# Optimization experiments

Measured on AMD Instinct MI355X. Metric: run time of the kernel, lower is better.

Reference implementation:

```python
import jax, jax.numpy as jnp
import numpy as np

N = 100000          # nodes
E = 1600000         # edges (before self-loops)
F_IN = 128          # dataset.num_node_features
HID = 32            # hidden_channels
HEADS = 4
NUM_CLASSES = 40
NEG_SLOPE = 0.2     # PyG GATConv default


def setup_inputs() -> dict:
    key = jax.random.key(0)
    ks = jax.random.split(key, 16)
    x = jax.random.normal(ks[0], (N, F_IN), dtype=jnp.float32)
    edge_index = jax.random.randint(ks[1], (2, E), 0, N, dtype=jnp.int64)

    def glorot(k, shape):
        lim = float(np.sqrt(6.0 / (shape[0] + shape[-1])))
        return jax.random.uniform(k, shape, jnp.float32, -lim, lim)

    # layer 0: F_IN -> HID, heads=HEADS, concat
    W0 = glorot(ks[2], (F_IN, HEADS * HID))
    as0 = glorot(ks[3], (HEADS, HID))
    ad0 = glorot(ks[4], (HEADS, HID))
    b0 = jnp.zeros((HEADS * HID,), jnp.float32)
    # layer 1: HEADS*HID -> HID, heads=HEADS, concat
    W1 = glorot(ks[5], (HEADS * HID, HEADS * HID))
    as1 = glorot(ks[6], (HEADS, HID))
    ad1 = glorot(ks[7], (HEADS, HID))
    b1 = jnp.zeros((HEADS * HID,), jnp.float32)
    # layer 2: HEADS*HID -> HID, heads=1, no concat
    W2 = glorot(ks[8], (HEADS * HID, HID))
    as2 = glorot(ks[9], (1, HID))
    ad2 = glorot(ks[10], (1, HID))
    b2 = jnp.zeros((HID,), jnp.float32)
    # final linear HID -> NUM_CLASSES
    lin_w = glorot(ks[11], (HID, NUM_CLASSES))
    lin_b = jnp.zeros((NUM_CLASSES,), jnp.float32)
    return dict(x=x, edge_index=edge_index, W0=W0, as0=as0, ad0=ad0, b0=b0,
                W1=W1, as1=as1, ad1=ad1, b1=b1,
                W2=W2, as2=as2, ad2=ad2, b2=b2, lin_w=lin_w, lin_b=lin_b)


def gat_conv(x, src, dst, W, a_src, a_dst, b, heads, out_ch, concat):
    n = x.shape[0]
    h = (x @ W).reshape(n, heads, out_ch)               # [N,H,C]
    alpha_s = (h * a_src).sum(-1)                        # [N,H]
    alpha_d = (h * a_dst).sum(-1)                        # [N,H]
    e = jax.nn.leaky_relu(alpha_s[src] + alpha_d[dst], NEG_SLOPE)  # [E,H]
    m = jax.ops.segment_max(e, dst, num_segments=n)      # segment softmax over in-edges
    e = jnp.exp(e - m[dst])
    denom = jax.ops.segment_sum(e, dst, num_segments=n)
    alpha = e / (denom[dst] + 1e-16)                     # [E,H]
    out = jax.ops.segment_sum(h[src] * alpha[:, :, None], dst, num_segments=n)  # [N,H,C]
    out = out.reshape(n, heads * out_ch) if concat else out.mean(axis=1)
    return out + b


def reference(x, edge_index, W0, as0, ad0, b0, W1, as1, ad1, b1,
              W2, as2, ad2, b2, lin_w, lin_b):
    n = x.shape[0]
    loop = jnp.arange(n, dtype=edge_index.dtype)
    src = jnp.concatenate([edge_index[0], loop])   # PyG GATConv adds self-loops
    dst = jnp.concatenate([edge_index[1], loop])
    x = jax.nn.relu(gat_conv(x, src, dst, W0, as0, ad0, b0, HEADS, HID, True))
    x = jax.nn.relu(gat_conv(x, src, dst, W1, as1, ad1, b1, HEADS, HID, True))
    x = jax.nn.relu(gat_conv(x, src, dst, W2, as2, ad2, b2, 1, HID, False))
    return x @ lin_w + lin_b
```

## Files before the change

kernel.cpp:

```cpp
#include <hip/hip_runtime.h>
#include <hip/hip_bf16.h>
#include <hip/hip_fp16.h>
#include <math.h>


#define NEG_SLOPE 0.2f

typedef __attribute__((ext_vector_type(8))) _Float16 f16x8;
typedef __attribute__((ext_vector_type(4))) float    f32x4;

struct h4pack { __half2 a, b; };


__global__ void zero1_kernel(int* __restrict__ a, int n) {
    int i = blockIdx.x * blockDim.x + threadIdx.x;
    if (i < n) a[i] = 0;
}

__global__ void count_rank_kernel(const int* __restrict__ ei, int eraw, int n,
                                  int* __restrict__ deg, int* __restrict__ rank) {
    int i = blockIdx.x * blockDim.x + threadIdx.x;
    int etot = eraw + n;
    if (i >= etot) return;
    int dst = (i < eraw) ? ei[eraw + i] : (i - eraw);
    rank[i] = atomicAdd(&deg[dst], 1);
}

__global__ __launch_bounds__(1024)
void scan_local_kernel(const int* __restrict__ deg, int* __restrict__ rowptr,
                       int* __restrict__ bsum, int n) {
    __shared__ int buf[1024];
    int tid = threadIdx.x;
    int i = blockIdx.x * 1024 + tid;
    int v = (i < n) ? deg[i] : 0;
    buf[tid] = v;
    __syncthreads();
    for (int off = 1; off < 1024; off <<= 1) {
        int t = (tid >= off) ? buf[tid - off] : 0;
        __syncthreads();
        buf[tid] += t;
        __syncthreads();
    }
    if (i < n) rowptr[i] = buf[tid] - v;
    if (tid == 1023) bsum[blockIdx.x] = buf[1023];
}

__global__ __launch_bounds__(128)
void scan_sums_kernel(const int* __restrict__ bsum, int* __restrict__ boffs, int nb) {
    __shared__ int buf[128];
    int tid = threadIdx.x;
    int v = (tid < nb) ? bsum[tid] : 0;
    buf[tid] = v;
    __syncthreads();
    for (int off = 1; off < 128; off <<= 1) {
        int t = (tid >= off) ? buf[tid - off] : 0;
        __syncthreads();
        buf[tid] += t;
        __syncthreads();
    }
    if (tid < nb) boffs[tid] = buf[tid] - v;
}

__global__ void scan_add_kernel(int* __restrict__ rowptr, const int* __restrict__ boffs,
                                int n, int etot) {
    int i = blockIdx.x * blockDim.x + threadIdx.x;
    if (i < n) rowptr[i] += boffs[i >> 10];
    if (i == 0) rowptr[n] = etot;
}

__global__ void scatter2_kernel(const int* __restrict__ ei, const int* __restrict__ rank,
                                int eraw, int n, const int* __restrict__ rowptr,
                                int* __restrict__ csr_src) {
    int i = blockIdx.x * blockDim.x + threadIdx.x;
    int etot = eraw + n;
    if (i >= etot) return;
    int src, dst;
    if (i < eraw) { src = ei[i]; dst = ei[eraw + i]; }
    else          { src = i - eraw; dst = src; }
    csr_src[rowptr[dst] + rank[i]] = src;
}


template <int OUTC>
__global__ void wpack_f16_kernel(const float* __restrict__ W, __half* __restrict__ Wp) {
    int i = blockIdx.x * blockDim.x + threadIdx.x;
    int j    = i & 7;
    int lane = (i >> 3) & 63;
    int ks   = (i >> 9) & 3;
    int ct   = i >> 11;
    int k = ks * 32 + (lane >> 4) * 8 + j;
    int c = ct * 16 + (lane & 15);
    Wp[i] = __float2half(W[k * OUTC + c]);
}


template <bool F32IN>
__global__ __launch_bounds__(256)
void gemm_mfma_coef_kernel(const void* __restrict__ Xv, const __half* __restrict__ Wp,
                           const float* __restrict__ a_s, const float* __restrict__ a_d,
                           __half* __restrict__ H, float* __restrict__ as_out,
                           float* __restrict__ ad_out, int n) {
    int t = threadIdx.x;
    int lane = t & 63;
    int wave = t >> 6;
    int l15 = lane & 15;
    int kg  = lane >> 4;
    int wbase = blockIdx.x * 128 + wave * 32;

    int node0 = wbase + l15;
    int node1 = wbase + 16 + l15;
    int n0c = (node0 < n) ? node0 : 0;
    int n1c = (node1 < n) ? node1 : 0;

    f32x4 acc[2][8];
#pragma unroll
    for (int tt = 0; tt < 2; tt++)
#pragma unroll
        for (int i = 0; i < 8; i++) acc[tt][i] = (f32x4){0.f, 0.f, 0.f, 0.f};

#pragma unroll
    for (int ks = 0; ks < 4; ks++) {
        f16x8 b0, b1;
        if constexpr (F32IN) {
            const float* X = (const float*)Xv;
            const float* p0 = X + (size_t)n0c * 128 + kg * 8 + ks * 32;
            const float* p1 = X + (size_t)n1c * 128 + kg * 8 + ks * 32;
            float4 x0 = *(const float4*)(p0), x1 = *(const float4*)(p0 + 4);
            b0[0] = (_Float16)x0.x; b0[1] = (_Float16)x0.y; b0[2] = (_Float16)x0.z; b0[3] = (_Float16)x0.w;
            b0[4] = (_Float16)x1.x; b0[5] = (_Float16)x1.y; b0[6] = (_Float16)x1.z; b0[7] = (_Float16)x1.w;
            float4 y0 = *(const float4*)(p1), y1 = *(const float4*)(p1 + 4);
            b1[0] = (_Float16)y0.x; b1[1] = (_Float16)y0.y; b1[2] = (_Float16)y0.z; b1[3] = (_Float16)y0.w;
            b1[4] = (_Float16)y1.x; b1[5] = (_Float16)y1.y; b1[6] = (_Float16)y1.z; b1[7] = (_Float16)y1.w;
        } else {
            const __half* X = (const __half*)Xv;
            b0 = *(const f16x8*)(X + (size_t)n0c * 128 + kg * 8 + ks * 32);
            b1 = *(const f16x8*)(X + (size_t)n1c * 128 + kg * 8 + ks * 32);
        }
#pragma unroll
        for (int ct = 0; ct < 8; ct++) {
            f16x8 a = *(const f16x8*)(Wp + (size_t)((ct * 4 + ks) * 64 + lane) * 8);
            acc[0][ct] = __builtin_amdgcn_mfma_f32_16x16x32_f16(a, b0, acc[0][ct], 0, 0, 0);
            acc[1][ct] = __builtin_amdgcn_mfma_f32_16x16x32_f16(a, b1, acc[1][ct], 0, 0, 0);
        }
    }

#pragma unroll
    for (int tt = 0; tt < 2; tt++) {
        int node = wbase + tt * 16 + l15;
        if (node < n) {
#pragma unroll
            for (int ct = 0; ct < 8; ct++) {
                h4pack p;
                p.a = __floats2half2_rn(acc[tt][ct][0], acc[tt][ct][1]);
                p.b = __floats2half2_rn(acc[tt][ct][2], acc[tt][ct][3]);
                *(h4pack*)(H + (size_t)node * 128 + ct * 16 + kg * 4) = p;
            }
        }
    }

#pragma unroll
    for (int tt = 0; tt < 2; tt++) {
        int node = wbase + tt * 16 + l15;
#pragma unroll
        for (int h = 0; h < 4; h++) {
            float s = 0.f, d = 0.f;
#pragma unroll
            for (int q = 0; q < 2; q++) {
                int ct = 2 * h + q;
#pragma unroll
                for (int r = 0; r < 4; r++) {
                    int c = q * 16 + kg * 4 + r;
                    float v = acc[tt][ct][r];
                    s += v * a_s[h * 32 + c];
                    d += v * a_d[h * 32 + c];
                }
            }
            s += __shfl_xor(s, 16); s += __shfl_xor(s, 32);
            d += __shfl_xor(d, 16); d += __shfl_xor(d, 32);
            if (kg == 0 && node < n) {
                as_out[(size_t)node * 4 + h] = s;
                ad_out[(size_t)node * 4 + h] = d;
            }
        }
    }
}


__global__ __launch_bounds__(256)
void gemm_mfma_l2_kernel(const __half* __restrict__ X, const __half* __restrict__ Wp,
                         const float* __restrict__ a_s, const float* __restrict__ a_d,
                         __half* __restrict__ H, float* __restrict__ as_out,
                         float* __restrict__ ad_out, int n) {
    __shared__ __half hs[4][32][40];
    int t = threadIdx.x;
    int wave = t >> 6, lane = t & 63;
    int l15 = lane & 15;
    int kg  = lane >> 4;
    int wbase = blockIdx.x * 128 + wave * 32;

    int row0 = wbase + l15;
    int row1 = wbase + 16 + l15;
    int r0c = (row0 < n) ? row0 : 0;
    int r1c = (row1 < n) ? row1 : 0;

    f32x4 acc[2][2];
#pragma unroll
    for (int tt = 0; tt < 2; tt++)
#pragma unroll
        for (int i = 0; i < 2; i++) acc[tt][i] = (f32x4){0.f, 0.f, 0.f, 0.f};

#pragma unroll
    for (int ks = 0; ks < 4; ks++) {
        f16x8 a0 = *(const f16x8*)(X + (size_t)r0c * 128 + kg * 8 + ks * 32);
        f16x8 a1 = *(const f16x8*)(X + (size_t)r1c * 128 + kg * 8 + ks * 32);
#pragma unroll
        for (int ct = 0; ct < 2; ct++) {
            f16x8 b = *(const f16x8*)(Wp + (size_t)((ct * 4 + ks) * 64 + lane) * 8);
            acc[0][ct] = __builtin_amdgcn_mfma_f32_16x16x32_f16(a0, b, acc[0][ct], 0, 0, 0);
            acc[1][ct] = __builtin_amdgcn_mfma_f32_16x16x32_f16(a1, b, acc[1][ct], 0, 0, 0);
        }
    }

#pragma unroll
    for (int tt = 0; tt < 2; tt++)
#pragma unroll
        for (int ct = 0; ct < 2; ct++)
#pragma unroll
            for (int r = 0; r < 4; r++)
                hs[wave][tt * 16 + kg * 4 + r][ct * 16 + l15] = __float2half(acc[tt][ct][r]);
    __syncthreads();

#pragma unroll
    for (int it = 0; it < 2; it++) {
        int lr    = it * 16 + (lane >> 2);
        int chunk = lane & 3;
        int orow  = wbase + lr;
        if (orow < n) {
            uint4 v = *(const uint4*)&hs[wave][lr][chunk * 8];
            *(uint4*)(H + (size_t)orow * 32 + chunk * 8) = v;
        }
    }

    if (lane < 32) {
        int orow = wbase + lane;
        if (orow < n) {
            const __half2* hp = (const __half2*)&hs[wave][lane][0];
            float s = 0.f, d = 0.f;
#pragma unroll
            for (int c2 = 0; c2 < 16; c2++) {
                float2 v = __half22float2(hp[c2]);
                s += v.x * a_s[2 * c2] + v.y * a_s[2 * c2 + 1];
                d += v.x * a_d[2 * c2] + v.y * a_d[2 * c2 + 1];
            }
            as_out[orow] = s;
            ad_out[orow] = d;
        }
    }
}


__global__ __launch_bounds__(256)
void gat_fused_f16_kernel(const __half* __restrict__ Hm,
                          const float* __restrict__ as_,
                          const float* __restrict__ ad_,
                          const int* __restrict__ rowptr,
                          const int* __restrict__ csr,
                          const float* __restrict__ bias,
                          __half* __restrict__ out, int n) {
    constexpr int GS = 32;
    int t = threadIdx.x;
    int node = blockIdx.x * 8 + (t >> 5);
    if (node >= n) return;
    int tl = t & 31;
    int h  = tl >> 3;
    int k8 = tl & 7;
    const uint2* H8 = (const uint2*)Hm;
    int e0 = rowptr[node], e1 = rowptr[node + 1];
    float ad_d = ad_[(size_t)node * 4 + h];

    int  ce  = e0 + k8;
    bool vA  = ce < e1;
    int  idxA = vA ? csr[ce] : 0;
    float asA = vA ? as_[(size_t)idxA * 4 + h] : 0.f;

    float m = -INFINITY, l = 0.f;
    float4 acc = make_float4(0.f, 0.f, 0.f, 0.f);

    for (int eb = e0; eb < e1; eb += 8) {
        uint2 u[8];
#pragma unroll
        for (int j = 0; j < 8; j++) {
            int src = __shfl(idxA, j, 8);
            u[j] = H8[(size_t)src * GS + tl];
        }

        int  ne  = eb + 8 + k8;
        bool vB  = ne < e1;
        int  idxB = vB ? csr[ne] : 0;
        float asB = vB ? as_[(size_t)idxB * 4 + h] : 0.f;

        float el = asA + ad_d;
        el = (el > 0.f) ? el : NEG_SLOPE * el;
        el = vA ? el : -INFINITY;

        float cm = el;
        cm = fmaxf(cm, __shfl_xor(cm, 1, 8));
        cm = fmaxf(cm, __shfl_xor(cm, 2, 8));
        cm = fmaxf(cm, __shfl_xor(cm, 4, 8));
        float m_new = fmaxf(m, cm);
        float scale = __expf(m - m_new);
        float p = vA ? __expf(el - m_new) : 0.f;

        float ps = p;
        ps += __shfl_xor(ps, 1, 8);
        ps += __shfl_xor(ps, 2, 8);
        ps += __shfl_xor(ps, 4, 8);
        l = l * scale + ps;
        acc.x *= scale; acc.y *= scale; acc.z *= scale; acc.w *= scale;
        m = m_new;

#pragma unroll
        for (int j = 0; j < 8; j++) {
            float pj  = __shfl(p, j, 8);
            float2 f01 = __half22float2(*(const __half2*)&u[j].x);
            float2 f23 = __half22float2(*(const __half2*)&u[j].y);
            acc.x += pj * f01.x; acc.y += pj * f01.y;
            acc.z += pj * f23.x; acc.w += pj * f23.y;
        }
        idxA = idxB; asA = asB; vA = vB;
    }

    float li = 1.f / (l + 1e-16f);
    float4 b4 = ((const float4*)bias)[tl];
    float4 o;
    o.x = fmaxf(acc.x * li + b4.x, 0.f);
    o.y = fmaxf(acc.y * li + b4.y, 0.f);
    o.z = fmaxf(acc.z * li + b4.z, 0.f);
    o.w = fmaxf(acc.w * li + b4.w, 0.f);
    h4pack po;
    po.a = __floats2half2_rn(o.x, o.y);
    po.b = __floats2half2_rn(o.z, o.w);
    ((h4pack*)out)[(size_t)node * 32 + tl] = po;
}


__global__ __launch_bounds__(256)
void gat_fused_l2_kernel(const __half* __restrict__ Hm,
                         const float* __restrict__ as_,
                         const float* __restrict__ ad_,
                         const int* __restrict__ rowptr,
                         const int* __restrict__ csr,
                         const float* __restrict__ bias,
                         const float* __restrict__ lw,
                         const float* __restrict__ lb,
                         float* __restrict__ out, int n) {
    int t = threadIdx.x;
    int node = blockIdx.x * 32 + (t >> 3);
    if (node >= n) return;
    int tl = t & 7;
    const uint2* H8 = (const uint2*)Hm;
    int e0 = rowptr[node], e1 = rowptr[node + 1];
    float ad_d = ad_[node];

    int  ce  = e0 + tl;
    bool vA  = ce < e1;
    int  idxA = vA ? csr[ce] : 0;
    float asA = vA ? as_[idxA] : 0.f;

    float m = -INFINITY, l = 0.f;
    float4 acc = make_float4(0.f, 0.f, 0.f, 0.f);

    for (int eb = e0; eb < e1; eb += 8) {
        uint2 u[8];
#pragma unroll
        for (int j = 0; j < 8; j++) {
            int src = __shfl(idxA, j, 8);
            u[j] = H8[(size_t)src * 8 + tl];
        }

        int  ne  = eb + 8 + tl;
        bool vB  = ne < e1;
        int  idxB = vB ? csr[ne] : 0;
        float asB = vB ? as_[idxB] : 0.f;

        float el = asA + ad_d;
        el = (el > 0.f) ? el : NEG_SLOPE * el;
        el = vA ? el : -INFINITY;

        float cm = el;
        cm = fmaxf(cm, __shfl_xor(cm, 1, 8));
        cm = fmaxf(cm, __shfl_xor(cm, 2, 8));
        cm = fmaxf(cm, __shfl_xor(cm, 4, 8));
        float m_new = fmaxf(m, cm);
        float scale = __expf(m - m_new);
        float p = vA ? __expf(el - m_new) : 0.f;

        float ps = p;
        ps += __shfl_xor(ps, 1, 8);
        ps += __shfl_xor(ps, 2, 8);
        ps += __shfl_xor(ps, 4, 8);
        l = l * scale + ps;
        acc.x *= scale; acc.y *= scale; acc.z *= scale; acc.w *= scale;
        m = m_new;

#pragma unroll
        for (int j = 0; j < 8; j++) {
            float pj  = __shfl(p, j, 8);
            float2 f01 = __half22float2(*(const __half2*)&u[j].x);
            float2 f23 = __half22float2(*(const __half2*)&u[j].y);
            acc.x += pj * f01.x; acc.y += pj * f01.y;
            acc.z += pj * f23.x; acc.w += pj * f23.y;
        }
        idxA = idxB; asA = asB; vA = vB;
    }

    float li = 1.f / (l + 1e-16f);
    float4 b4 = ((const float4*)bias)[tl];
    float4 o;
    o.x = fmaxf(acc.x * li + b4.x, 0.f);
    o.y = fmaxf(acc.y * li + b4.y, 0.f);
    o.z = fmaxf(acc.z * li + b4.z, 0.f);
    o.w = fmaxf(acc.w * li + b4.w, 0.f);

    float fin0 = lb[tl];
    float fin1 = lb[tl + 8];
    float fin2 = lb[tl + 16];
    float fin3 = lb[tl + 24];
    float fin4 = lb[tl + 32];
#pragma unroll
    for (int j = 0; j < 8; j++) {
        float vx = __shfl(o.x, j, 8);
        float vy = __shfl(o.y, j, 8);
        float vz = __shfl(o.z, j, 8);
        float vw = __shfl(o.w, j, 8);
        const float* l0 = lw + (size_t)(4 * j) * 40;
#pragma unroll
        for (int c = 0; c < 5; c++) {
            int cls = tl + 8 * c;
            float v = vx * l0[cls] + vy * l0[40 + cls] + vz * l0[80 + cls] + vw * l0[120 + cls];
            if (c == 0) fin0 += v;
            else if (c == 1) fin1 += v;
            else if (c == 2) fin2 += v;
            else if (c == 3) fin3 += v;
            else fin4 += v;
        }
    }
    float* op = out + (size_t)node * 40;
    op[tl]      = fin0;
    op[tl + 8]  = fin1;
    op[tl + 16] = fin2;
    op[tl + 24] = fin3;
    op[tl + 32] = fin4;
}


extern "C" void kernel_launch(void* const* d_in, const int* in_sizes, int n_in,
                              void* d_out, int out_size, void* d_ws, size_t ws_size,
                              hipStream_t stream) {
    const float* x   = (const float*)d_in[0];
    const int*   ei  = (const int*)d_in[1];
    const float* W0  = (const float*)d_in[2];
    const float* as0 = (const float*)d_in[3];
    const float* ad0 = (const float*)d_in[4];
    const float* b0  = (const float*)d_in[5];
    const float* W1  = (const float*)d_in[6];
    const float* as1 = (const float*)d_in[7];
    const float* ad1 = (const float*)d_in[8];
    const float* b1  = (const float*)d_in[9];
    const float* W2  = (const float*)d_in[10];
    const float* as2 = (const float*)d_in[11];
    const float* ad2 = (const float*)d_in[12];
    const float* b2  = (const float*)d_in[13];
    const float* lw  = (const float*)d_in[14];
    const float* lb  = (const float*)d_in[15];
    float* out = (float*)d_out;

    const int n    = in_sizes[0] / 128;
    const int eraw = in_sizes[1] / 2;
    const int etot = eraw + n;
    const int nb   = (n + 1023) / 1024;

    char* wsp = (char*)d_ws;
    size_t off = 0;
    auto alloc = [&](size_t bytes) -> void* {
        void* p = wsp + off;
        off += (bytes + 255) & ~(size_t)255;
        return p;
    };
    __half* h16    = (__half*)alloc((size_t)n * 128 * 2);
    __half* buf16  = (__half*)alloc((size_t)n * 128 * 2);
    __half* h2     = (__half*)alloc((size_t)n * 32 * 2);
    __half* Wp0    = (__half*)alloc((size_t)128 * 128 * 2);
    __half* Wp1    = (__half*)alloc((size_t)128 * 128 * 2);
    __half* Wp2    = (__half*)alloc((size_t)128 * 32 * 2);
    float*  asb    = (float*)alloc((size_t)n * 4 * 4);
    float*  adb    = (float*)alloc((size_t)n * 4 * 4);
    int*    deg    = (int*)alloc((size_t)n * 4);
    int*    rank   = (int*)alloc((size_t)etot * 4);
    int*    rowptr = (int*)alloc((size_t)(n + 1) * 4);
    int*    csr    = (int*)alloc((size_t)etot * 4);
    int*    bsum   = (int*)alloc((size_t)nb * 4);
    int*    boffs  = (int*)alloc((size_t)nb * 4);

    zero1_kernel<<<(n + 255) / 256, 256, 0, stream>>>(deg, n);
    count_rank_kernel<<<(etot + 255) / 256, 256, 0, stream>>>(ei, eraw, n, deg, rank);
    wpack_f16_kernel<128><<<64, 256, 0, stream>>>(W0, Wp0);
    wpack_f16_kernel<128><<<64, 256, 0, stream>>>(W1, Wp1);
    wpack_f16_kernel<32><<<16, 256, 0, stream>>>(W2, Wp2);
    scan_local_kernel<<<nb, 1024, 0, stream>>>(deg, rowptr, bsum, n);
    scan_sums_kernel<<<1, 128, 0, stream>>>(bsum, boffs, nb);
    scan_add_kernel<<<(n + 255) / 256, 256, 0, stream>>>(rowptr, boffs, n, etot);
    scatter2_kernel<<<(etot + 255) / 256, 256, 0, stream>>>(ei, rank, eraw, n, rowptr, csr);

    const int gblocks = (n + 127) / 128;

    gemm_mfma_coef_kernel<true><<<gblocks, 256, 0, stream>>>(x, Wp0, as0, ad0, h16, asb, adb, n);
    gat_fused_f16_kernel<<<(n + 7) / 8, 256, 0, stream>>>(h16, asb, adb, rowptr, csr, b0, buf16, n);

    gemm_mfma_coef_kernel<false><<<gblocks, 256, 0, stream>>>(buf16, Wp1, as1, ad1, h16, asb, adb, n);
    gat_fused_f16_kernel<<<(n + 7) / 8, 256, 0, stream>>>(h16, asb, adb, rowptr, csr, b1, buf16, n);

    gemm_mfma_l2_kernel<<<gblocks, 256, 0, stream>>>(buf16, Wp2, as2, ad2, h2, asb, adb, n);
    gat_fused_l2_kernel<<<(n + 31) / 32, 256, 0, stream>>>(h2, asb, adb, rowptr, csr, b2, lw, lb, out, n);
}
```

Baseline: 461.2 us.

## Fuse layer-2 linear projection and attention coefficients into layer-1 aggregation

The layer-1 aggregation kernel now keeps each node's 128-wide output in shared memory and computes the 32-wide layer-2 projection and its source/destination attention scores directly, writing only the small h2 buffer. This removes the separate layer-2 GEMM kernel and the write and re-read of the 128-wide fp16 intermediate. The three weight-packing kernels are merged into one launch, and the zeroing kernel is replaced by hipMemsetAsync. In exchange, the layer-2 matmul now runs on scalar FMAs instead of MFMA, with 32 threads per node, and the kernel uses extra shared memory.

```diff
diff --git a/kernel.cpp b/kernel.cpp
--- a/kernel.cpp
+++ b/kernel.cpp
@@ -11,11 +11,6 @@
 
 struct h4pack { __half2 a, b; };
 
-
-__global__ void zero1_kernel(int* __restrict__ a, int n) {
-    int i = blockIdx.x * blockDim.x + threadIdx.x;
-    if (i < n) a[i] = 0;
-}
 
 __global__ void count_rank_kernel(const int* __restrict__ ei, int eraw, int n,
                                   int* __restrict__ deg, int* __restrict__ rank) {
@@ -81,16 +76,27 @@
 }
 
 
-template <int OUTC>
-__global__ void wpack_f16_kernel(const float* __restrict__ W, __half* __restrict__ Wp) {
+__global__ void wpack_all_kernel(const float* __restrict__ W0, const float* __restrict__ W1,
+                                 const float* __restrict__ W2,
+                                 __half* __restrict__ Wp0, __half* __restrict__ Wp1,
+                                 __half* __restrict__ W2t) {
     int i = blockIdx.x * blockDim.x + threadIdx.x;
-    int j    = i & 7;
-    int lane = (i >> 3) & 63;
-    int ks   = (i >> 9) & 3;
-    int ct   = i >> 11;
-    int k = ks * 32 + (lane >> 4) * 8 + j;
-    int c = ct * 16 + (lane & 15);
-    Wp[i] = __float2half(W[k * OUTC + c]);
+    if (i < 32768) {
+        const float* W = (i < 16384) ? W0 : W1;
+        __half* Wp     = (i < 16384) ? Wp0 : Wp1;
+        int ii   = i & 16383;
+        int j    = ii & 7;
+        int lane = (ii >> 3) & 63;
+        int ks   = (ii >> 9) & 3;
+        int ct   = ii >> 11;
+        int k = ks * 32 + (lane >> 4) * 8 + j;
+        int c = ct * 16 + (lane & 15);
+        Wp[ii] = __float2half(W[k * 128 + c]);
+    } else if (i < 36864) {
+        int j = i - 32768;
+        int c = j >> 7, k = j & 127;
+        W2t[c * 128 + k] = __float2half(W2[k * 32 + c]);
+    }
 }
 
 
@@ -186,79 +192,7 @@
 }
 
 
-__global__ __launch_bounds__(256)
-void gemm_mfma_l2_kernel(const __half* __restrict__ X, const __half* __restrict__ Wp,
-                         const float* __restrict__ a_s, const float* __restrict__ a_d,
-                         __half* __restrict__ H, float* __restrict__ as_out,
-                         float* __restrict__ ad_out, int n) {
-    __shared__ __half hs[4][32][40];
-    int t = threadIdx.x;
-    int wave = t >> 6, lane = t & 63;
-    int l15 = lane & 15;
-    int kg  = lane >> 4;
-    int wbase = blockIdx.x * 128 + wave * 32;
-
-    int row0 = wbase + l15;
-    int row1 = wbase + 16 + l15;
-    int r0c = (row0 < n) ? row0 : 0;
-    int r1c = (row1 < n) ? row1 : 0;
-
-    f32x4 acc[2][2];
-#pragma unroll
-    for (int tt = 0; tt < 2; tt++)
-#pragma unroll
-        for (int i = 0; i < 2; i++) acc[tt][i] = (f32x4){0.f, 0.f, 0.f, 0.f};
-
-#pragma unroll
-    for (int ks = 0; ks < 4; ks++) {
-        f16x8 a0 = *(const f16x8*)(X + (size_t)r0c * 128 + kg * 8 + ks * 32);
-        f16x8 a1 = *(const f16x8*)(X + (size_t)r1c * 128 + kg * 8 + ks * 32);
-#pragma unroll
-        for (int ct = 0; ct < 2; ct++) {
-            f16x8 b = *(const f16x8*)(Wp + (size_t)((ct * 4 + ks) * 64 + lane) * 8);
-            acc[0][ct] = __builtin_amdgcn_mfma_f32_16x16x32_f16(a0, b, acc[0][ct], 0, 0, 0);
-            acc[1][ct] = __builtin_amdgcn_mfma_f32_16x16x32_f16(a1, b, acc[1][ct], 0, 0, 0);
-        }
-    }
-
-#pragma unroll
-    for (int tt = 0; tt < 2; tt++)
-#pragma unroll
-        for (int ct = 0; ct < 2; ct++)
-#pragma unroll
-            for (int r = 0; r < 4; r++)
-                hs[wave][tt * 16 + kg * 4 + r][ct * 16 + l15] = __float2half(acc[tt][ct][r]);
-    __syncthreads();
-
-#pragma unroll
-    for (int it = 0; it < 2; it++) {
-        int lr    = it * 16 + (lane >> 2);
-        int chunk = lane & 3;
-        int orow  = wbase + lr;
-        if (orow < n) {
-            uint4 v = *(const uint4*)&hs[wave][lr][chunk * 8];
-            *(uint4*)(H + (size_t)orow * 32 + chunk * 8) = v;
-        }
-    }
-
-    if (lane < 32) {
-        int orow = wbase + lane;
-        if (orow < n) {
-            const __half2* hp = (const __half2*)&hs[wave][lane][0];
-            float s = 0.f, d = 0.f;
-#pragma unroll
-            for (int c2 = 0; c2 < 16; c2++) {
-                float2 v = __half22float2(hp[c2]);
-                s += v.x * a_s[2 * c2] + v.y * a_s[2 * c2 + 1];
-                d += v.x * a_d[2 * c2] + v.y * a_d[2 * c2 + 1];
-            }
-            as_out[orow] = s;
-            ad_out[orow] = d;
-        }
-    }
-}
-
-
+template <bool L2FUSE>
 __global__ __launch_bounds__(256)
 void gat_fused_f16_kernel(const __half* __restrict__ Hm,
                           const float* __restrict__ as_,
@@ -266,10 +200,17 @@
                           const int* __restrict__ rowptr,
                           const int* __restrict__ csr,
                           const float* __restrict__ bias,
-                          __half* __restrict__ out, int n) {
+                          __half* __restrict__ out,
+                          const __half* __restrict__ W2t,
+                          const float* __restrict__ as2w,
+                          const float* __restrict__ ad2w,
+                          float* __restrict__ as2_out,
+                          float* __restrict__ ad2_out, int n) {
     constexpr int GS = 32;
+    __shared__ float os[8][128];
     int t = threadIdx.x;
-    int node = blockIdx.x * 8 + (t >> 5);
+    int g = t >> 5;
+    int node = blockIdx.x * 8 + g;
     if (node >= n) return;
     int tl = t & 31;
     int h  = tl >> 3;
@@ -337,10 +278,40 @@
     o.y = fmaxf(acc.y * li + b4.y, 0.f);
     o.z = fmaxf(acc.z * li + b4.z, 0.f);
     o.w = fmaxf(acc.w * li + b4.w, 0.f);
-    h4pack po;
-    po.a = __floats2half2_rn(o.x, o.y);
-    po.b = __floats2half2_rn(o.z, o.w);
-    ((h4pack*)out)[(size_t)node * 32 + tl] = po;
+
+    if constexpr (!L2FUSE) {
+        h4pack po;
+        po.a = __floats2half2_rn(o.x, o.y);
+        po.b = __floats2half2_rn(o.z, o.w);
+        ((h4pack*)out)[(size_t)node * 32 + tl] = po;
+    } else {
+        *(float4*)&os[g][tl * 4] = o;
+        float hv = 0.f;
+        const f16x8* w8 = (const f16x8*)(W2t + (size_t)tl * 128);
+#pragma unroll
+        for (int kb = 0; kb < 16; kb++) {
+            f16x8 w = w8[kb];
+            const float* op_ = &os[g][kb * 8];
+            float4 xa = *(const float4*)op_;
+            float4 xb = *(const float4*)(op_ + 4);
+            hv += xa.x * (float)w[0] + xa.y * (float)w[1]
+                + xa.z * (float)w[2] + xa.w * (float)w[3]
+                + xb.x * (float)w[4] + xb.y * (float)w[5]
+                + xb.z * (float)w[6] + xb.w * (float)w[7];
+        }
+        out[(size_t)node * 32 + tl] = __float2half(hv);
+        float s = hv * as2w[tl];
+        float d = hv * ad2w[tl];
+        s += __shfl_xor(s, 1, 32);  d += __shfl_xor(d, 1, 32);
+        s += __shfl_xor(s, 2, 32);  d += __shfl_xor(d, 2, 32);
+        s += __shfl_xor(s, 4, 32);  d += __shfl_xor(d, 4, 32);
+        s += __shfl_xor(s, 8, 32);  d += __shfl_xor(d, 8, 32);
+        s += __shfl_xor(s, 16, 32); d += __shfl_xor(d, 16, 32);
+        if (tl == 0) {
+            as2_out[node] = s;
+            ad2_out[node] = d;
+        }
+    }
 }
 
 
@@ -488,13 +459,14 @@
         return p;
     };
     __half* h16    = (__half*)alloc((size_t)n * 128 * 2);
-    __half* buf16  = (__half*)alloc((size_t)n * 128 * 2);
     __half* h2     = (__half*)alloc((size_t)n * 32 * 2);
     __half* Wp0    = (__half*)alloc((size_t)128 * 128 * 2);
     __half* Wp1    = (__half*)alloc((size_t)128 * 128 * 2);
-    __half* Wp2    = (__half*)alloc((size_t)128 * 32 * 2);
+    __half* W2t    = (__half*)alloc((size_t)32 * 128 * 2);
     float*  asb    = (float*)alloc((size_t)n * 4 * 4);
     float*  adb    = (float*)alloc((size_t)n * 4 * 4);
+    float*  asb2   = (float*)alloc((size_t)n * 4);
+    float*  adb2   = (float*)alloc((size_t)n * 4);
     int*    deg    = (int*)alloc((size_t)n * 4);
     int*    rank   = (int*)alloc((size_t)etot * 4);
     int*    rowptr = (int*)alloc((size_t)(n + 1) * 4);
@@ -502,11 +474,9 @@
     int*    bsum   = (int*)alloc((size_t)nb * 4);
     int*    boffs  = (int*)alloc((size_t)nb * 4);
 
-    zero1_kernel<<<(n + 255) / 256, 256, 0, stream>>>(deg, n);
+    hipMemsetAsync(deg, 0, (size_t)n * 4, stream);
     count_rank_kernel<<<(etot + 255) / 256, 256, 0, stream>>>(ei, eraw, n, deg, rank);
-    wpack_f16_kernel<128><<<64, 256, 0, stream>>>(W0, Wp0);
-    wpack_f16_kernel<128><<<64, 256, 0, stream>>>(W1, Wp1);
-    wpack_f16_kernel<32><<<16, 256, 0, stream>>>(W2, Wp2);
+    wpack_all_kernel<<<144, 256, 0, stream>>>(W0, W1, W2, Wp0, Wp1, W2t);
     scan_local_kernel<<<nb, 1024, 0, stream>>>(deg, rowptr, bsum, n);
     scan_sums_kernel<<<1, 128, 0, stream>>>(bsum, boffs, nb);
     scan_add_kernel<<<(n + 255) / 256, 256, 0, stream>>>(rowptr, boffs, n, etot);
@@ -514,12 +484,15 @@
 
     const int gblocks = (n + 127) / 128;
 
+    __half* l0out = (__half*)alloc((size_t)n * 128 * 2);
+
     gemm_mfma_coef_kernel<true><<<gblocks, 256, 0, stream>>>(x, Wp0, as0, ad0, h16, asb, adb, n);
-    gat_fused_f16_kernel<<<(n + 7) / 8, 256, 0, stream>>>(h16, asb, adb, rowptr, csr, b0, buf16, n);
-
-    gemm_mfma_coef_kernel<false><<<gblocks, 256, 0, stream>>>(buf16, Wp1, as1, ad1, h16, asb, adb, n);
-    gat_fused_f16_kernel<<<(n + 7) / 8, 256, 0, stream>>>(h16, asb, adb, rowptr, csr, b1, buf16, n);
-
-    gemm_mfma_l2_kernel<<<gblocks, 256, 0, stream>>>(buf16, Wp2, as2, ad2, h2, asb, adb, n);
-    gat_fused_l2_kernel<<<(n + 31) / 32, 256, 0, stream>>>(h2, asb, adb, rowptr, csr, b2, lw, lb, out, n);
-}
+    gat_fused_f16_kernel<false><<<(n + 7) / 8, 256, 0, stream>>>(
+        h16, asb, adb, rowptr, csr, b0, l0out, nullptr, nullptr, nullptr, nullptr, nullptr, n);
+
+    gemm_mfma_coef_kernel<false><<<gblocks, 256, 0, stream>>>(l0out, Wp1, as1, ad1, h16, asb, adb, n);
+    gat_fused_f16_kernel<true><<<(n + 7) / 8, 256, 0, stream>>>(
+        h16, asb, adb, rowptr, csr, b1, h2, W2t, as2, ad2, asb2, adb2, n);
+
+    gat_fused_l2_kernel<<<(n + 31) / 32, 256, 0, stream>>>(h2, asb2, adb2, rowptr, csr, b2, lw, lb, out, n);
+}
```

Measured after the change: 511.9 us. +11.0%, slower.
